# Kernel optimization log

Hardware: AMD Instinct MI355X
Metric: run time of the kernel (lower is better)

Reference implementation:

```python
import jax, jax.numpy as jnp
import numpy as np

N = 50000   # nodes per graph
E = 800000  # edges per graph
D = 128     # in_dim (num_features)
H = 128     # hidden_channels
R = 8       # num_etypes


def setup_inputs() -> dict:
    key = jax.random.key(0)
    ks = jax.random.split(key, 32)
    inp = {}
    inp["x1"] = jax.random.normal(ks[0], (N, D), dtype=jnp.float32)
    inp["edge_index1"] = jax.random.randint(ks[1], (2, E), 0, N)
    inp["edge_type1"] = jnp.sort(jax.random.randint(ks[2], (E,), 0, R))
    inp["x2"] = jax.random.normal(ks[3], (N, D), dtype=jnp.float32)
    inp["edge_index2"] = jax.random.randint(ks[4], (2, E), 0, N)
    inp["edge_type2"] = jnp.sort(jax.random.randint(ks[5], (E,), 0, R))
    # RGCNConv params: relation weights [R, in, out], root weight [in, out], bias [out]
    dims = [(D, H), (H, H), (H, H)]
    k = 6
    for l, (di, do) in enumerate(dims):
        s = 1.0 / np.sqrt(di)
        inp[f"W{l}"] = jax.random.normal(ks[k], (R, di, do), dtype=jnp.float32) * s; k += 1
        inp[f"root{l}"] = jax.random.normal(ks[k], (di, do), dtype=jnp.float32) * s; k += 1
        inp[f"bias{l}"] = jnp.zeros((do,), dtype=jnp.float32)
    # FCL: MLP on concat(u1, u2) of width 2*H -> H -> 1 (assumed architecture)
    s = 1.0 / np.sqrt(2 * H)
    inp["fc1_w"] = jax.random.normal(ks[k], (2 * H, H), dtype=jnp.float32) * s; k += 1
    inp["fc1_b"] = jnp.zeros((H,), dtype=jnp.float32)
    s = 1.0 / np.sqrt(H)
    inp["fc2_w"] = jax.random.normal(ks[k], (H, 1), dtype=jnp.float32) * s; k += 1
    inp["fc2_b"] = jnp.zeros((1,), dtype=jnp.float32)
    return inp


def rgcn_conv(x, src, dst, etype, W, root, bias):
    # PyG RGCNConv: out_i = root @ x_i + bias + sum_r mean_{j in N_r(i)} W_r x_j
    # transform all nodes by all relation weights: [R, N, H]
    t = jnp.einsum('nd,rdh->rnh', x, W)
    msg = t[etype, src]                       # [E, H] per-edge gathered messages
    comb = dst * R + etype                    # combined (node, relation) segment id
    cnt = jax.ops.segment_sum(jnp.ones((E,), x.dtype), comb, num_segments=N * R)
    msg = msg * (1.0 / jnp.maximum(cnt, 1.0))[comb][:, None]  # per-relation mean norm
    agg = jax.ops.segment_sum(msg, dst, num_segments=N)       # scatter-add over relations
    return agg + x @ root + bias


def gnn(x, edge_index, edge_type, params):
    src, dst = edge_index[0], edge_index[1]
    u = jax.nn.relu(rgcn_conv(x, src, dst, edge_type, *params[0]))
    u = jax.nn.relu(rgcn_conv(u, src, dst, edge_type, *params[1]))
    u = rgcn_conv(u, src, dst, edge_type, *params[2])
    return jnp.mean(u, axis=0).reshape(1, -1)  # [1, H]


def reference(x1, edge_index1, edge_type1, x2, edge_index2, edge_type2,
              W0, root0, bias0, W1, root1, bias1, W2, root2, bias2,
              fc1_w, fc1_b, fc2_w, fc2_b):
    params = [(W0, root0, bias0), (W1, root1, bias1), (W2, root2, bias2)]
    u1 = gnn(x1, edge_index1, edge_type1, params)
    u2 = gnn(x2, edge_index2, edge_type2, params)
    h = jnp.concatenate([u1, u2], axis=-1)    # [1, 2H]
    return jax.nn.relu(h @ fc1_w + fc1_b) @ fc2_w + fc2_b  # [1, 1]
```

## Files before the change

kernel.cpp:

```cpp
#include <hip/hip_runtime.h>

#define R_ET 8
#define DH 128

typedef __bf16 bf16x8 __attribute__((ext_vector_type(8)));
typedef float f32x4 __attribute__((ext_vector_type(4)));
typedef ushort u16x8 __attribute__((ext_vector_type(8)));

__device__ __forceinline__ ushort f2bf(float f) {
  unsigned u = __float_as_uint(f);
  u += 0x7fff + ((u >> 16) & 1);
  return (ushort)(u >> 16);
}

__global__ void count_kernel(const int* __restrict__ ei, const int* __restrict__ et,
                             int* __restrict__ cnt, int E) {
  int e = blockIdx.x * blockDim.x + threadIdx.x;
  if (e < E) atomicAdd(&cnt[ei[E + e] * R_ET + et[e]], 1);
}

__global__ __launch_bounds__(1024) void scan1_kernel(const int* __restrict__ cnt,
                                                     int* __restrict__ off,
                                                     int* __restrict__ bsum, int M) {
  __shared__ int s[1024];
  int tid = threadIdx.x;
  int i = blockIdx.x * 1024 + tid;
  int d = (i < M) ? cnt[i] : 0;
  s[tid] = d;
  __syncthreads();
  for (int step = 1; step < 1024; step <<= 1) {
    int v = (tid >= step) ? s[tid - step] : 0;
    __syncthreads();
    s[tid] += v;
    __syncthreads();
  }
  if (i < M) off[i] = s[tid] - d;
  if (tid == 1023) bsum[blockIdx.x] = s[1023];
}

__global__ __launch_bounds__(1024) void scan2_kernel(int* __restrict__ bsum, int nb) {
  __shared__ int s[1024];
  int tid = threadIdx.x;
  int v = (tid < nb) ? bsum[tid] : 0;
  s[tid] = v;
  __syncthreads();
  for (int step = 1; step < 1024; step <<= 1) {
    int x = (tid >= step) ? s[tid - step] : 0;
    __syncthreads();
    s[tid] += x;
    __syncthreads();
  }
  if (tid < nb) bsum[tid] = s[tid] - v;
}

__global__ __launch_bounds__(1024) void scan3_kernel(int* __restrict__ off,
                                                     int* __restrict__ cursor,
                                                     const int* __restrict__ bsum,
                                                     int M, int E) {
  int i = blockIdx.x * 1024 + threadIdx.x;
  if (i < M) {
    int o = off[i] + bsum[blockIdx.x];
    off[i] = o;
    cursor[i] = o;
  }
  if (i == 0) off[M] = E;
}

__global__ void place_kernel(const int* __restrict__ ei, const int* __restrict__ et,
                             int* __restrict__ cursor, int* __restrict__ meta, int E) {
  int e = blockIdx.x * blockDim.x + threadIdx.x;
  if (e >= E) return;
  int src = ei[e], dst = ei[E + e], r = et[e];
  int slot = atomicAdd(&cursor[dst * R_ET + r], 1);
  meta[slot] = src | (r << 28);
}

__global__ __launch_bounds__(256) void wconv_kernel(const float* __restrict__ root,
                                                    const float* __restrict__ W,
                                                    ushort* __restrict__ Wt) {
  int mat = blockIdx.x;
  const float* src = (mat == 8) ? root : (W + (size_t)mat * DH * DH);
  ushort* dst = Wt + (size_t)mat * DH * DH;
  for (int idx = threadIdx.x; idx < DH * DH; idx += 256) {
    int n = idx >> 7, k = idx & 127;
    dst[n * DH + (((k >> 3) ^ (n & 7)) << 3) + (k & 7)] = f2bf(src[k * DH + n]);
  }
}

__global__ __launch_bounds__(256) void aconv_kernel(const float* __restrict__ src,
                                                    ushort* __restrict__ dst,
                                                    int total, int padtotal) {
  int i4 = (blockIdx.x * 256 + threadIdx.x) * 4;
  if (i4 >= padtotal) return;
  int row = i4 >> 7, k = i4 & 127;
  ushort4 o = make_ushort4(0, 0, 0, 0);
  if (i4 < total) {
    float4 v = *(const float4*)&src[i4];
    o = make_ushort4(f2bf(v.x), f2bf(v.y), f2bf(v.z), f2bf(v.w));
  }
  *(ushort4*)&dst[(size_t)row * DH + (((k >> 3) ^ (row & 7)) << 3) + (k & 7)] = o;
}

__global__ __launch_bounds__(256) void gemm_mfma(
    const ushort* __restrict__ Abf, const ushort* __restrict__ Wt,
    ushort* __restrict__ t, int Npad) {
  __shared__ ushort As[128 * DH];
  __shared__ ushort Bs[128 * DH];
  const int tid = threadIdx.x;
  const int wave = tid >> 6, lane = tid & 63;
  const int quad = lane >> 4, l15 = lane & 15;
  const int rbase = blockIdx.x * 128;
  const int wr = (wave >> 1) * 64, wc = (wave & 1) * 64;

  const ushort* gA = Abf + (size_t)rbase * DH;
#pragma unroll
  for (int it = 0; it < 8; it++) {
    __builtin_amdgcn_global_load_lds(
        (const __attribute__((address_space(1))) void*)(gA + (it * 256 + tid) * 8),
        (__attribute__((address_space(3))) void*)(As + (it * 256 + wave * 64) * 8), 16, 0, 0);
  }

  for (int m = 0; m < 3; m++) {
    const int mat = blockIdx.y * 3 + m;
    const ushort* gB = Wt + (size_t)mat * DH * DH;
    if (m) __syncthreads();
#pragma unroll
    for (int it = 0; it < 8; it++) {
      __builtin_amdgcn_global_load_lds(
          (const __attribute__((address_space(1))) void*)(gB + (it * 256 + tid) * 8),
          (__attribute__((address_space(3))) void*)(Bs + (it * 256 + wave * 64) * 8), 16, 0, 0);
    }
    __syncthreads();

    f32x4 acc[4][4];
#pragma unroll
    for (int i = 0; i < 4; i++)
#pragma unroll
      for (int j = 0; j < 4; j++) acc[i][j] = (f32x4){0.f, 0.f, 0.f, 0.f};

#pragma unroll
    for (int kc = 0; kc < 4; kc++) {
      bf16x8 af[4], bfr[4];
#pragma unroll
      for (int i = 0; i < 4; i++) {
        int ra = wr + i * 16 + l15;
        int rb = wc + i * 16 + l15;
        af[i] = *(const bf16x8*)&As[ra * DH + (((kc * 4 + quad) ^ (ra & 7)) << 3)];
        bfr[i] = *(const bf16x8*)&Bs[rb * DH + (((kc * 4 + quad) ^ (rb & 7)) << 3)];
      }
#pragma unroll
      for (int i = 0; i < 4; i++)
#pragma unroll
        for (int j = 0; j < 4; j++)
          acc[i][j] = __builtin_amdgcn_mfma_f32_16x16x32_bf16(af[i], bfr[j], acc[i][j], 0, 0, 0);
    }

    __syncthreads();
#pragma unroll
    for (int i = 0; i < 4; i++)
#pragma unroll
      for (int j = 0; j < 4; j++) {
        int col = wc + j * 16 + l15;
#pragma unroll
        for (int r = 0; r < 4; r++)
          Bs[(wr + i * 16 + quad * 4 + r) * DH + col] = f2bf(acc[i][j][r]);
      }
    __syncthreads();
    ushort* tp = t + ((size_t)mat * Npad + rbase) * DH;
#pragma unroll
    for (int c = 0; c < 8; c++) {
      u16x8 v = *(const u16x8*)&Bs[tid * 64 + c * 8];
      *(u16x8*)&tp[tid * 64 + c * 8] = v;
    }
  }
}

__device__ __forceinline__ void gather_accum(const int* __restrict__ meta,
                                             const ushort* __restrict__ t,
                                             int start, int end, int lane, int colb,
                                             float invl, int NpadS,
                                             float& ax, float& ay) {
  for (int base = start; base < end; base += 64) {
    int m = min(64, end - base);
    int md = (lane < m) ? meta[base + lane] : 0;
    int j = 0;
    for (; j + 4 <= m; j += 4) {
      int p0 = __shfl(md, j), p1 = __shfl(md, j + 1);
      int p2 = __shfl(md, j + 2), p3 = __shfl(md, j + 3);
      int r0 = (unsigned)p0 >> 28, r1 = (unsigned)p1 >> 28;
      int r2 = (unsigned)p2 >> 28, r3 = (unsigned)p3 >> 28;
      float s0 = __shfl(invl, r0), s1 = __shfl(invl, r1);
      float s2 = __shfl(invl, r2), s3 = __shfl(invl, r3);
      unsigned u0 = *(const unsigned*)&t[r0 * NpadS + ((p0 & 0x0fffffff) << 7) + colb];
      unsigned u1 = *(const unsigned*)&t[r1 * NpadS + ((p1 & 0x0fffffff) << 7) + colb];
      unsigned u2 = *(const unsigned*)&t[r2 * NpadS + ((p2 & 0x0fffffff) << 7) + colb];
      unsigned u3 = *(const unsigned*)&t[r3 * NpadS + ((p3 & 0x0fffffff) << 7) + colb];
      ax = fmaf(__uint_as_float(u0 << 16), s0, ax);
      ay = fmaf(__uint_as_float(u0 & 0xffff0000u), s0, ay);
      ax = fmaf(__uint_as_float(u1 << 16), s1, ax);
      ay = fmaf(__uint_as_float(u1 & 0xffff0000u), s1, ay);
      ax = fmaf(__uint_as_float(u2 << 16), s2, ax);
      ay = fmaf(__uint_as_float(u2 & 0xffff0000u), s2, ay);
      ax = fmaf(__uint_as_float(u3 << 16), s3, ax);
      ay = fmaf(__uint_as_float(u3 & 0xffff0000u), s3, ay);
    }
    for (; j < m; j++) {
      int pj = __shfl(md, j);
      int rj = (unsigned)pj >> 28;
      float sj = __shfl(invl, rj);
      unsigned u = *(const unsigned*)&t[rj * NpadS + ((pj & 0x0fffffff) << 7) + colb];
      ax = fmaf(__uint_as_float(u << 16), sj, ax);
      ay = fmaf(__uint_as_float(u & 0xffff0000u), sj, ay);
    }
  }
}

__global__ __launch_bounds__(256) void gather_mid(
    const int* __restrict__ off, const int* __restrict__ meta,
    const int* __restrict__ cnt, const ushort* __restrict__ t,
    const float* __restrict__ bias, ushort* __restrict__ Abf, int N, int Npad) {
  int dst = blockIdx.x * 4 + (threadIdx.x >> 6);
  if (dst >= N) return;
  int lane = threadIdx.x & 63, colb = lane * 2;
  int dst8 = dst * R_ET;
  int NpadS = Npad * DH;
  float invl = 1.f / (float)cnt[dst8 + (lane & 7)];
  float ax = 0.f, ay = 0.f;
  gather_accum(meta, t, off[dst8], off[dst8 + 8], lane, colb, invl, NpadS, ax, ay);
  unsigned u9 = *(const unsigned*)&t[8 * NpadS + (dst << 7) + colb];
  float2 bv = *(const float2*)&bias[colb];
  float rx = fmaxf(__uint_as_float(u9 << 16) + ax + bv.x, 0.f);
  float ry = fmaxf(__uint_as_float(u9 & 0xffff0000u) + ay + bv.y, 0.f);
  unsigned o = (unsigned)f2bf(rx) | ((unsigned)f2bf(ry) << 16);
  *(unsigned*)&Abf[(size_t)dst * DH + (((colb >> 3) ^ (dst & 7)) << 3) + (colb & 7)] = o;
}

__global__ __launch_bounds__(256) void gather_last(
    const int* __restrict__ off, const int* __restrict__ meta,
    const int* __restrict__ cnt, const ushort* __restrict__ t,
    float* __restrict__ upart, int N, int Npad) {
  __shared__ float sx[256], sy[256];
  int dst = blockIdx.x * 4 + (threadIdx.x >> 6);
  int lane = threadIdx.x & 63, colb = lane * 2;
  float px = 0.f, py = 0.f;
  if (dst < N) {
    int dst8 = dst * R_ET;
    int NpadS = Npad * DH;
    float invl = 1.f / (float)cnt[dst8 + (lane & 7)];
    float ax = 0.f, ay = 0.f;
    gather_accum(meta, t, off[dst8], off[dst8 + 8], lane, colb, invl, NpadS, ax, ay);
    unsigned u9 = *(const unsigned*)&t[8 * NpadS + (dst << 7) + colb];
    px = __uint_as_float(u9 << 16) + ax;
    py = __uint_as_float(u9 & 0xffff0000u) + ay;
  }
  sx[threadIdx.x] = px;
  sy[threadIdx.x] = py;
  __syncthreads();
  if (threadIdx.x < 64) {
    float tx = sx[threadIdx.x] + sx[64 + threadIdx.x] + sx[128 + threadIdx.x] + sx[192 + threadIdx.x];
    float ty = sy[threadIdx.x] + sy[64 + threadIdx.x] + sy[128 + threadIdx.x] + sy[192 + threadIdx.x];
    float* up = upart + (size_t)(blockIdx.x & 63) * DH;
    atomicAdd(&up[threadIdx.x * 2], tx);
    atomicAdd(&up[threadIdx.x * 2 + 1], ty);
  }
}

__global__ __launch_bounds__(256) void mlp_kernel(
    const float* __restrict__ upart, const float* __restrict__ bias2,
    const float* __restrict__ fc1w, const float* __restrict__ fc1b,
    const float* __restrict__ fc2w, const float* __restrict__ fc2b,
    float* __restrict__ out, int N) {
  __shared__ float uin[256];
  __shared__ float hred[128];
  int tid = threadIdx.x;
  {
    int g = tid >> 7, col = tid & 127;
    const float* up = upart + (size_t)g * 64 * DH + col;
    float s = 0.f;
#pragma unroll
    for (int p = 0; p < 64; p++) s += up[(size_t)p * DH];
    uin[tid] = s * (1.f / (float)N) + bias2[col];
  }
  __syncthreads();
  if (tid < 128) {
    float s = fc1b[tid];
    for (int i = 0; i < 256; i++) s = fmaf(uin[i], fc1w[i * 128 + tid], s);
    s = fmaxf(s, 0.f);
    hred[tid] = s * fc2w[tid];
  }
  __syncthreads();
  if (tid == 0) {
    float s = fc2b[0];
    for (int i = 0; i < 128; i++) s += hred[i];
    out[0] = s;
  }
}

extern "C" void kernel_launch(void* const* d_in, const int* in_sizes, int n_in,
                              void* d_out, int out_size, void* d_ws, size_t ws_size,
                              hipStream_t stream) {
  const float* x[2] = {(const float*)d_in[0], (const float*)d_in[3]};
  const int* ei[2] = {(const int*)d_in[1], (const int*)d_in[4]};
  const int* et[2] = {(const int*)d_in[2], (const int*)d_in[5]};
  const float* Wp[3] = {(const float*)d_in[6], (const float*)d_in[9], (const float*)d_in[12]};
  const float* rootp[3] = {(const float*)d_in[7], (const float*)d_in[10], (const float*)d_in[13]};
  const float* biasp[3] = {(const float*)d_in[8], (const float*)d_in[11], (const float*)d_in[14]};
  const float* fc1w = (const float*)d_in[15];
  const float* fc1b = (const float*)d_in[16];
  const float* fc2w = (const float*)d_in[17];
  const float* fc2b = (const float*)d_in[18];

  const int N = in_sizes[0] / DH;
  const int E = in_sizes[2];
  const int Npad = (N + 127) & ~127;
  const int M = N * R_ET;
  const int MB = (M + 1023) / 1024;

  char* ws = (char*)d_ws;
  size_t ob = 0;
  auto alloc = [&](size_t bytes) {
    void* p = ws + ob;
    ob = (ob + bytes + 255) & ~(size_t)255;
    return p;
  };
  int* cnt = (int*)alloc((size_t)M * 4);
  int* offs = (int*)alloc((size_t)(M + 1) * 4);
  int* cursor = (int*)alloc((size_t)M * 4);
  int* bsum = (int*)alloc(1024 * 4);
  int* meta = (int*)alloc((size_t)E * 4);
  float* upart = (float*)alloc((size_t)2 * 64 * DH * 4);
  ushort* Abf = (ushort*)alloc((size_t)Npad * DH * 2);
  ushort* Wt = (ushort*)alloc((size_t)3 * 9 * DH * DH * 2);
  ushort* tbuf = (ushort*)alloc((size_t)9 * Npad * DH * 2);
  (void)ws_size;

  hipMemsetAsync(upart, 0, (size_t)2 * 64 * DH * sizeof(float), stream);
  for (int l = 0; l < 3; l++)
    wconv_kernel<<<9, 256, 0, stream>>>(rootp[l], Wp[l], Wt + (size_t)l * 9 * DH * DH);

  dim3 ggrid(Npad / 128, 3);
  dim3 egrid((E + 255) / 256);
  const int total = N * DH, padtotal = Npad * DH;
  dim3 agrid((padtotal / 4 + 255) / 256);

  for (int g = 0; g < 2; g++) {
    hipMemsetAsync(cnt, 0, (size_t)M * sizeof(int), stream);
    count_kernel<<<egrid, 256, 0, stream>>>(ei[g], et[g], cnt, E);
    scan1_kernel<<<MB, 1024, 0, stream>>>(cnt, offs, bsum, M);
    scan2_kernel<<<1, 1024, 0, stream>>>(bsum, MB);
    scan3_kernel<<<MB, 1024, 0, stream>>>(offs, cursor, bsum, M, E);
    place_kernel<<<egrid, 256, 0, stream>>>(ei[g], et[g], cursor, meta, E);
    aconv_kernel<<<agrid, 256, 0, stream>>>(x[g], Abf, total, padtotal);
    for (int l = 0; l < 3; l++) {
      gemm_mfma<<<ggrid, 256, 0, stream>>>(Abf, Wt + (size_t)l * 9 * DH * DH, tbuf, Npad);
      if (l < 2) {
        gather_mid<<<(N + 3) / 4, 256, 0, stream>>>(offs, meta, cnt, tbuf, biasp[l],
                                                    Abf, N, Npad);
      } else {
        gather_last<<<(N + 3) / 4, 256, 0, stream>>>(offs, meta, cnt, tbuf,
                                                     upart + (size_t)g * 64 * DH, N, Npad);
      }
    }
  }
  mlp_kernel<<<1, 256, 0, stream>>>(upart, biasp[2], fc1w, fc1b, fc2w, fc2b,
                                    (float*)d_out, N);
}
```

Measured before the change: 896.5 us.

## Aggregate raw features per relation then multiply, fusing gather and GEMM per layer

Reorders each RGCN layer so neighbour features are mean-aggregated per (node, relation) in LDS first, then one 16x1152 by 1152x128 MFMA product covers all relations plus the root weight. Gather and GEMM become a single kernel per layer. This removes the 9xN transformed-feature buffer and its HBM write and read traffic. In exchange, the gather inner loop is no longer unrolled, each block streams the full 9-matrix weight set from global/L2, and bias and ReLU are folded into the epilogue.

```diff
diff --git a/kernel.cpp b/kernel.cpp
--- a/kernel.cpp
+++ b/kernel.cpp
@@ -2,10 +2,10 @@
 
 #define R_ET 8
 #define DH 128
+#define AS 1160
 
 typedef __bf16 bf16x8 __attribute__((ext_vector_type(8)));
 typedef float f32x4 __attribute__((ext_vector_type(4)));
-typedef ushort u16x8 __attribute__((ext_vector_type(8)));
 
 __device__ __forceinline__ ushort f2bf(float f) {
   unsigned u = __float_as_uint(f);
@@ -72,7 +72,7 @@
   if (e >= E) return;
   int src = ei[e], dst = ei[E + e], r = et[e];
   int slot = atomicAdd(&cursor[dst * R_ET + r], 1);
-  meta[slot] = src | (r << 28);
+  meta[slot] = src;
 }
 
 __global__ __launch_bounds__(256) void wconv_kernel(const float* __restrict__ root,
@@ -83,185 +83,116 @@
   ushort* dst = Wt + (size_t)mat * DH * DH;
   for (int idx = threadIdx.x; idx < DH * DH; idx += 256) {
     int n = idx >> 7, k = idx & 127;
-    dst[n * DH + (((k >> 3) ^ (n & 7)) << 3) + (k & 7)] = f2bf(src[k * DH + n]);
+    dst[n * DH + k] = f2bf(src[k * DH + n]);
   }
 }
 
 __global__ __launch_bounds__(256) void aconv_kernel(const float* __restrict__ src,
-                                                    ushort* __restrict__ dst,
-                                                    int total, int padtotal) {
+                                                    ushort* __restrict__ dst, int total) {
   int i4 = (blockIdx.x * 256 + threadIdx.x) * 4;
-  if (i4 >= padtotal) return;
-  int row = i4 >> 7, k = i4 & 127;
-  ushort4 o = make_ushort4(0, 0, 0, 0);
-  if (i4 < total) {
-    float4 v = *(const float4*)&src[i4];
-    o = make_ushort4(f2bf(v.x), f2bf(v.y), f2bf(v.z), f2bf(v.w));
-  }
-  *(ushort4*)&dst[(size_t)row * DH + (((k >> 3) ^ (row & 7)) << 3) + (k & 7)] = o;
-}
-
-__global__ __launch_bounds__(256) void gemm_mfma(
-    const ushort* __restrict__ Abf, const ushort* __restrict__ Wt,
-    ushort* __restrict__ t, int Npad) {
-  __shared__ ushort As[128 * DH];
-  __shared__ ushort Bs[128 * DH];
+  if (i4 >= total) return;
+  float4 v = *(const float4*)&src[i4];
+  *(ushort4*)&dst[i4] = make_ushort4(f2bf(v.x), f2bf(v.y), f2bf(v.z), f2bf(v.w));
+}
+
+template <int LAST>
+__global__ __launch_bounds__(256) void rgcn_fused(
+    const ushort* __restrict__ x, const ushort* __restrict__ Wt,
+    const int* __restrict__ offs, const int* __restrict__ meta,
+    const float* __restrict__ bias, ushort* __restrict__ xnext,
+    float* __restrict__ upart, int N, int M) {
+  __shared__ ushort agg[16 * AS];
   const int tid = threadIdx.x;
-  const int wave = tid >> 6, lane = tid & 63;
-  const int quad = lane >> 4, l15 = lane & 15;
-  const int rbase = blockIdx.x * 128;
-  const int wr = (wave >> 1) * 64, wc = (wave & 1) * 64;
-
-  const ushort* gA = Abf + (size_t)rbase * DH;
-#pragma unroll
-  for (int it = 0; it < 8; it++) {
-    __builtin_amdgcn_global_load_lds(
-        (const __attribute__((address_space(1))) void*)(gA + (it * 256 + tid) * 8),
-        (__attribute__((address_space(3))) void*)(As + (it * 256 + wave * 64) * 8), 16, 0, 0);
-  }
-
-  for (int m = 0; m < 3; m++) {
-    const int mat = blockIdx.y * 3 + m;
-    const ushort* gB = Wt + (size_t)mat * DH * DH;
-    if (m) __syncthreads();
-#pragma unroll
-    for (int it = 0; it < 8; it++) {
-      __builtin_amdgcn_global_load_lds(
-          (const __attribute__((address_space(1))) void*)(gB + (it * 256 + tid) * 8),
-          (__attribute__((address_space(3))) void*)(Bs + (it * 256 + wave * 64) * 8), 16, 0, 0);
-    }
-    __syncthreads();
-
-    f32x4 acc[4][4];
-#pragma unroll
-    for (int i = 0; i < 4; i++)
-#pragma unroll
-      for (int j = 0; j < 4; j++) acc[i][j] = (f32x4){0.f, 0.f, 0.f, 0.f};
-
-#pragma unroll
-    for (int kc = 0; kc < 4; kc++) {
-      bf16x8 af[4], bfr[4];
-#pragma unroll
-      for (int i = 0; i < 4; i++) {
-        int ra = wr + i * 16 + l15;
-        int rb = wc + i * 16 + l15;
-        af[i] = *(const bf16x8*)&As[ra * DH + (((kc * 4 + quad) ^ (ra & 7)) << 3)];
-        bfr[i] = *(const bf16x8*)&Bs[rb * DH + (((kc * 4 + quad) ^ (rb & 7)) << 3)];
+  const int wid = tid >> 6, lane = tid & 63;
+
+  {
+    uint* az = (uint*)&agg[(wid * 4) * AS];
+    for (int i = lane; i < 4 * AS / 2; i += 64) az[i] = 0;
+  }
+
+  const int dst0 = blockIdx.x * 16 + wid * 4;
+  const int s0 = dst0 * R_ET;
+  int offreg = offs[min(s0 + min(lane, 64), M)];
+  int estart = __shfl(offreg, 0);
+  int eend = __shfl(offreg, 32);
+  int cur = 0;
+  int curstart = estart;
+  int nxt = __shfl(offreg, 1);
+  float sx = 0.f, sy = 0.f;
+  for (int base = estart; base < eend; base += 64) {
+    int mm = min(64, eend - base);
+    int md = (lane < mm) ? meta[base + lane] : 0;
+    for (int j = 0; j < mm; j++) {
+      int slot = base + j;
+      while (slot >= nxt) {
+        int cnt = nxt - curstart;
+        if (cnt > 0) {
+          float inv = 1.f / (float)cnt;
+          int dloc = wid * 4 + (cur >> 3);
+          int r = cur & 7;
+          *(uint*)&agg[dloc * AS + r * DH + lane * 2] =
+              (uint)f2bf(sx * inv) | ((uint)f2bf(sy * inv) << 16);
+        }
+        sx = sy = 0.f;
+        cur++;
+        curstart = nxt;
+        nxt = __shfl(offreg, min(cur + 1, 32));
       }
-#pragma unroll
-      for (int i = 0; i < 4; i++)
-#pragma unroll
-        for (int j = 0; j < 4; j++)
-          acc[i][j] = __builtin_amdgcn_mfma_f32_16x16x32_bf16(af[i], bfr[j], acc[i][j], 0, 0, 0);
-    }
-
-    __syncthreads();
-#pragma unroll
-    for (int i = 0; i < 4; i++)
-#pragma unroll
-      for (int j = 0; j < 4; j++) {
-        int col = wc + j * 16 + l15;
-#pragma unroll
-        for (int r = 0; r < 4; r++)
-          Bs[(wr + i * 16 + quad * 4 + r) * DH + col] = f2bf(acc[i][j][r]);
+      int src = __shfl(md, j);
+      unsigned u = *(const unsigned*)&x[src * DH + lane * 2];
+      sx += __uint_as_float(u << 16);
+      sy += __uint_as_float(u & 0xffff0000u);
+    }
+  }
+  {
+    int cnt = nxt - curstart;
+    if (cnt > 0) {
+      float inv = 1.f / (float)cnt;
+      int dloc = wid * 4 + (cur >> 3);
+      int r = cur & 7;
+      *(uint*)&agg[dloc * AS + r * DH + lane * 2] =
+          (uint)f2bf(sx * inv) | ((uint)f2bf(sy * inv) << 16);
+    }
+  }
+#pragma unroll
+  for (int d = 0; d < 4; d++) {
+    int dst = dst0 + d;
+    if (dst < N) {
+      unsigned u = *(const unsigned*)&x[(size_t)dst * DH + lane * 2];
+      *(uint*)&agg[(wid * 4 + d) * AS + 8 * DH + lane * 2] = u;
+    }
+  }
+  __syncthreads();
+
+  const int l15 = lane & 15, quad = lane >> 4;
+  for (int c = 0; c < 2; c++) {
+    int ct = wid * 2 + c;
+    int col = ct * 16 + l15;
+    f32x4 acc = (f32x4){0.f, 0.f, 0.f, 0.f};
+#pragma unroll
+    for (int r = 0; r < 9; r++) {
+      const ushort* wb = Wt + ((size_t)r << 14) + col * DH + quad * 8;
+      const ushort* ab = &agg[l15 * AS + r * DH + quad * 8];
+#pragma unroll
+      for (int kc = 0; kc < 4; kc++) {
+        bf16x8 a = *(const bf16x8*)&ab[kc * 32];
+        bf16x8 b = *(const bf16x8*)&wb[kc * 32];
+        acc = __builtin_amdgcn_mfma_f32_16x16x32_bf16(a, b, acc, 0, 0, 0);
       }
-    __syncthreads();
-    ushort* tp = t + ((size_t)mat * Npad + rbase) * DH;
-#pragma unroll
-    for (int c = 0; c < 8; c++) {
-      u16x8 v = *(const u16x8*)&Bs[tid * 64 + c * 8];
-      *(u16x8*)&tp[tid * 64 + c * 8] = v;
-    }
-  }
-}
-
-__device__ __forceinline__ void gather_accum(const int* __restrict__ meta,
-                                             const ushort* __restrict__ t,
-                                             int start, int end, int lane, int colb,
-                                             float invl, int NpadS,
-                                             float& ax, float& ay) {
-  for (int base = start; base < end; base += 64) {
-    int m = min(64, end - base);
-    int md = (lane < m) ? meta[base + lane] : 0;
-    int j = 0;
-    for (; j + 4 <= m; j += 4) {
-      int p0 = __shfl(md, j), p1 = __shfl(md, j + 1);
-      int p2 = __shfl(md, j + 2), p3 = __shfl(md, j + 3);
-      int r0 = (unsigned)p0 >> 28, r1 = (unsigned)p1 >> 28;
-      int r2 = (unsigned)p2 >> 28, r3 = (unsigned)p3 >> 28;
-      float s0 = __shfl(invl, r0), s1 = __shfl(invl, r1);
-      float s2 = __shfl(invl, r2), s3 = __shfl(invl, r3);
-      unsigned u0 = *(const unsigned*)&t[r0 * NpadS + ((p0 & 0x0fffffff) << 7) + colb];
-      unsigned u1 = *(const unsigned*)&t[r1 * NpadS + ((p1 & 0x0fffffff) << 7) + colb];
-      unsigned u2 = *(const unsigned*)&t[r2 * NpadS + ((p2 & 0x0fffffff) << 7) + colb];
-      unsigned u3 = *(const unsigned*)&t[r3 * NpadS + ((p3 & 0x0fffffff) << 7) + colb];
-      ax = fmaf(__uint_as_float(u0 << 16), s0, ax);
-      ay = fmaf(__uint_as_float(u0 & 0xffff0000u), s0, ay);
-      ax = fmaf(__uint_as_float(u1 << 16), s1, ax);
-      ay = fmaf(__uint_as_float(u1 & 0xffff0000u), s1, ay);
-      ax = fmaf(__uint_as_float(u2 << 16), s2, ax);
-      ay = fmaf(__uint_as_float(u2 & 0xffff0000u), s2, ay);
-      ax = fmaf(__uint_as_float(u3 << 16), s3, ax);
-      ay = fmaf(__uint_as_float(u3 & 0xffff0000u), s3, ay);
-    }
-    for (; j < m; j++) {
-      int pj = __shfl(md, j);
-      int rj = (unsigned)pj >> 28;
-      float sj = __shfl(invl, rj);
-      unsigned u = *(const unsigned*)&t[rj * NpadS + ((pj & 0x0fffffff) << 7) + colb];
-      ax = fmaf(__uint_as_float(u << 16), sj, ax);
-      ay = fmaf(__uint_as_float(u & 0xffff0000u), sj, ay);
-    }
-  }
-}
-
-__global__ __launch_bounds__(256) void gather_mid(
-    const int* __restrict__ off, const int* __restrict__ meta,
-    const int* __restrict__ cnt, const ushort* __restrict__ t,
-    const float* __restrict__ bias, ushort* __restrict__ Abf, int N, int Npad) {
-  int dst = blockIdx.x * 4 + (threadIdx.x >> 6);
-  if (dst >= N) return;
-  int lane = threadIdx.x & 63, colb = lane * 2;
-  int dst8 = dst * R_ET;
-  int NpadS = Npad * DH;
-  float invl = 1.f / (float)cnt[dst8 + (lane & 7)];
-  float ax = 0.f, ay = 0.f;
-  gather_accum(meta, t, off[dst8], off[dst8 + 8], lane, colb, invl, NpadS, ax, ay);
-  unsigned u9 = *(const unsigned*)&t[8 * NpadS + (dst << 7) + colb];
-  float2 bv = *(const float2*)&bias[colb];
-  float rx = fmaxf(__uint_as_float(u9 << 16) + ax + bv.x, 0.f);
-  float ry = fmaxf(__uint_as_float(u9 & 0xffff0000u) + ay + bv.y, 0.f);
-  unsigned o = (unsigned)f2bf(rx) | ((unsigned)f2bf(ry) << 16);
-  *(unsigned*)&Abf[(size_t)dst * DH + (((colb >> 3) ^ (dst & 7)) << 3) + (colb & 7)] = o;
-}
-
-__global__ __launch_bounds__(256) void gather_last(
-    const int* __restrict__ off, const int* __restrict__ meta,
-    const int* __restrict__ cnt, const ushort* __restrict__ t,
-    float* __restrict__ upart, int N, int Npad) {
-  __shared__ float sx[256], sy[256];
-  int dst = blockIdx.x * 4 + (threadIdx.x >> 6);
-  int lane = threadIdx.x & 63, colb = lane * 2;
-  float px = 0.f, py = 0.f;
-  if (dst < N) {
-    int dst8 = dst * R_ET;
-    int NpadS = Npad * DH;
-    float invl = 1.f / (float)cnt[dst8 + (lane & 7)];
-    float ax = 0.f, ay = 0.f;
-    gather_accum(meta, t, off[dst8], off[dst8 + 8], lane, colb, invl, NpadS, ax, ay);
-    unsigned u9 = *(const unsigned*)&t[8 * NpadS + (dst << 7) + colb];
-    px = __uint_as_float(u9 << 16) + ax;
-    py = __uint_as_float(u9 & 0xffff0000u) + ay;
-  }
-  sx[threadIdx.x] = px;
-  sy[threadIdx.x] = py;
-  __syncthreads();
-  if (threadIdx.x < 64) {
-    float tx = sx[threadIdx.x] + sx[64 + threadIdx.x] + sx[128 + threadIdx.x] + sx[192 + threadIdx.x];
-    float ty = sy[threadIdx.x] + sy[64 + threadIdx.x] + sy[128 + threadIdx.x] + sy[192 + threadIdx.x];
-    float* up = upart + (size_t)(blockIdx.x & 63) * DH;
-    atomicAdd(&up[threadIdx.x * 2], tx);
-    atomicAdd(&up[threadIdx.x * 2 + 1], ty);
+    }
+    if (!LAST) {
+      float bv = bias[col];
+#pragma unroll
+      for (int reg = 0; reg < 4; reg++) {
+        int dst = blockIdx.x * 16 + quad * 4 + reg;
+        if (dst < N) xnext[(size_t)dst * DH + col] = f2bf(fmaxf(acc[reg] + bv, 0.f));
+      }
+    } else {
+      float v = acc[0] + acc[1] + acc[2] + acc[3];
+      v += __shfl_xor(v, 16);
+      v += __shfl_xor(v, 32);
+      if (quad == 0) atomicAdd(&upart[(blockIdx.x & 63) * DH + col], v);
+    }
   }
 }
 
@@ -312,7 +243,6 @@
 
   const int N = in_sizes[0] / DH;
   const int E = in_sizes[2];
-  const int Npad = (N + 127) & ~127;
   const int M = N * R_ET;
   const int MB = (M + 1023) / 1024;
 
@@ -329,19 +259,18 @@
   int* bsum = (int*)alloc(1024 * 4);
   int* meta = (int*)alloc((size_t)E * 4);
   float* upart = (float*)alloc((size_t)2 * 64 * DH * 4);
-  ushort* Abf = (ushort*)alloc((size_t)Npad * DH * 2);
+  ushort* A0 = (ushort*)alloc((size_t)N * DH * 2);
+  ushort* A1 = (ushort*)alloc((size_t)N * DH * 2);
   ushort* Wt = (ushort*)alloc((size_t)3 * 9 * DH * DH * 2);
-  ushort* tbuf = (ushort*)alloc((size_t)9 * Npad * DH * 2);
   (void)ws_size;
 
   hipMemsetAsync(upart, 0, (size_t)2 * 64 * DH * sizeof(float), stream);
   for (int l = 0; l < 3; l++)
     wconv_kernel<<<9, 256, 0, stream>>>(rootp[l], Wp[l], Wt + (size_t)l * 9 * DH * DH);
 
-  dim3 ggrid(Npad / 128, 3);
   dim3 egrid((E + 255) / 256);
-  const int total = N * DH, padtotal = Npad * DH;
-  dim3 agrid((padtotal / 4 + 255) / 256);
+  const int total = N * DH;
+  const int nblk = (N + 15) / 16;
 
   for (int g = 0; g < 2; g++) {
     hipMemsetAsync(cnt, 0, (size_t)M * sizeof(int), stream);
@@ -350,17 +279,14 @@
     scan2_kernel<<<1, 1024, 0, stream>>>(bsum, MB);
     scan3_kernel<<<MB, 1024, 0, stream>>>(offs, cursor, bsum, M, E);
     place_kernel<<<egrid, 256, 0, stream>>>(ei[g], et[g], cursor, meta, E);
-    aconv_kernel<<<agrid, 256, 0, stream>>>(x[g], Abf, total, padtotal);
-    for (int l = 0; l < 3; l++) {
-      gemm_mfma<<<ggrid, 256, 0, stream>>>(Abf, Wt + (size_t)l * 9 * DH * DH, tbuf, Npad);
-      if (l < 2) {
-        gather_mid<<<(N + 3) / 4, 256, 0, stream>>>(offs, meta, cnt, tbuf, biasp[l],
-                                                    Abf, N, Npad);
-      } else {
-        gather_last<<<(N + 3) / 4, 256, 0, stream>>>(offs, meta, cnt, tbuf,
-                                                     upart + (size_t)g * 64 * DH, N, Npad);
-      }
-    }
+    aconv_kernel<<<(total / 4 + 255) / 256, 256, 0, stream>>>(x[g], A0, total);
+    rgcn_fused<0><<<nblk, 256, 0, stream>>>(A0, Wt + 0 * 9 * DH * DH, offs, meta,
+                                            biasp[0], A1, nullptr, N, M);
+    rgcn_fused<0><<<nblk, 256, 0, stream>>>(A1, Wt + 1 * 9 * DH * DH, offs, meta,
+                                            biasp[1], A0, nullptr, N, M);
+    rgcn_fused<1><<<nblk, 256, 0, stream>>>(A0, Wt + 2 * 9 * DH * DH, offs, meta,
+                                            nullptr, nullptr, upart + (size_t)g * 64 * DH,
+                                            N, M);
   }
   mlp_kernel<<<1, 256, 0, stream>>>(upart, biasp[2], fc1w, fc1b, fc2w, fc2b,
                                     (float*)d_out, N);
```

Measured after the change: 1.638 ms. 82.8% more time.
